# Kernel optimization log

Hardware: AMD Instinct MI355X
Metric: run time of the kernel (lower is better)

Reference implementation:

```python
import jax, jax.numpy as jnp
import numpy as np

B, S, D = 4, 2048, 1024
H, HD = 16, 64
MLP = 4 * D
EPS = 1e-6


def _rms_norm(x, scale):
    var = jnp.mean(jnp.square(x), axis=-1, keepdims=True)
    return x * jax.lax.rsqrt(var + EPS) * scale


def setup_inputs() -> dict:
    key = jax.random.key(0)
    ks = jax.random.split(key, 8)
    sd = D ** -0.5
    return {
        "x": jax.random.normal(ks[0], (B, S, D), jnp.float32),
        "pre_norm_scale": jnp.ones((D,), jnp.float32),
        "w_mlp_in": jax.random.normal(ks[1], (D, MLP), jnp.float32) * sd,   # MLPBlockInput, no bias
        "wq": jax.random.normal(ks[2], (D, H, HD), jnp.float32) * sd,
        "wk": jax.random.normal(ks[3], (D, H, HD), jnp.float32) * sd,
        "wv": jax.random.normal(ks[4], (D, H, HD), jnp.float32) * sd,
        "w_mlp_out": jax.random.normal(ks[5], (MLP, D), jnp.float32) * (MLP ** -0.5),
        "b_mlp_out": jnp.zeros((D,), jnp.float32),
        "w_attn_out": jax.random.normal(ks[6], (H, HD, D), jnp.float32) * sd,  # DenseGeneral axis=(-2,-1)
        "b_attn_out": jnp.zeros((D,), jnp.float32),
    }


def reference(x, pre_norm_scale, w_mlp_in, wq, wk, wv, w_mlp_out, b_mlp_out,
              w_attn_out, b_attn_out):
    residual = x
    xn = _rms_norm(x, pre_norm_scale)                      # pre_norm (TPNorm)

    # QKVMLPDense: fused MLP-input + QKV projections
    h = jax.nn.gelu(jnp.einsum("bsd,df->bsf", xn, w_mlp_in))   # [B,S,MLP]
    q = jnp.einsum("bsd,dhk->bshk", xn, wq)                    # [B,S,H,HD]
    k = jnp.einsum("bsd,dhk->bshk", xn, wk)
    v = jnp.einsum("bsd,dhk->bshk", xn, wv)

    # dot_product_attention (mask=None)
    scores = jnp.einsum("bqhd,bkhd->bhqk", q, k) / jnp.sqrt(jnp.asarray(HD, x.dtype))
    probs = jax.nn.softmax(scores, axis=-1)
    attn_v = jnp.einsum("bhqk,bkhd->bqhd", probs, v)           # [B,S,H,HD]

    # AttnMLPOut: mlp_out + attn_out
    mlp_out = jnp.einsum("bsf,fd->bsd", h, w_mlp_out) + b_mlp_out
    attn_out = jnp.einsum("bqhk,hkd->bqd", attn_v, w_attn_out) + b_attn_out
    block_out = mlp_out + attn_out                              # dropout is identity (train=False)
    return residual + block_out
```

## Files before the change

### kernel.cpp

```cpp
#include <hip/hip_runtime.h>
#include <cstdint>
#include <cstddef>

typedef float floatx4 __attribute__((ext_vector_type(4)));
typedef short bf16x8 __attribute__((ext_vector_type(8)));

#define MFMA(a, b, c) __builtin_amdgcn_mfma_f32_16x16x32_bf16((a), (b), (c), 0, 0, 0)

__device__ __forceinline__ unsigned short f2bf(float f) {
  union { float f; unsigned int u; } v; v.f = f;
  unsigned int u = v.u;
  unsigned int r = (u + 0x7FFFu + ((u >> 16) & 1u)) >> 16;
  return (unsigned short)r;
}

__device__ __forceinline__ void gload_lds16(const unsigned short* g, unsigned short* s) {
  __builtin_amdgcn_global_load_lds(
      (const __attribute__((address_space(1))) unsigned int*)g,
      (__attribute__((address_space(3))) unsigned int*)s, 16, 0, 0);
}

__device__ __forceinline__ float gelu_f(float v) {
  float z = 0.7978845608028654f * (v + 0.044715f * v * v * v);
  float e = __expf(2.0f * z);
  float th = 1.0f - 2.0f / (e + 1.0f);
  return 0.5f * v * (1.0f + th);
}

__global__ __launch_bounds__(256) void prep_all(
    const float* __restrict__ w_mlp_in, const float* __restrict__ wq,
    const float* __restrict__ wk, const float* __restrict__ wv,
    const float* __restrict__ w_mlp_out, const float* __restrict__ w_attn_out,
    const float* __restrict__ x, const float* __restrict__ pns,
    unsigned short* __restrict__ wcatT, unsigned short* __restrict__ wcat2T,
    unsigned short* __restrict__ xn) {
  __shared__ float tile[32][33];
  __shared__ float ws4[4];
  int id = blockIdx.x;
  if (id >= 12288) {
    int row = id - 12288;
    const float4 v = ((const float4*)(x + (size_t)row * 1024))[threadIdx.x];
    float ss = v.x * v.x + v.y * v.y + v.z * v.z + v.w * v.w;
#pragma unroll
    for (int off = 1; off < 64; off <<= 1) ss += __shfl_xor(ss, off, 64);
    if ((threadIdx.x & 63) == 0) ws4[threadIdx.x >> 6] = ss;
    __syncthreads();
    float tot = ws4[0] + ws4[1] + ws4[2] + ws4[3];
    float rs = rsqrtf(tot * (1.0f / 1024.0f) + 1e-6f);
    const float4 sc = ((const float4*)pns)[threadIdx.x];
    uint2 o;
    o.x = (unsigned)f2bf(v.x * rs * sc.x) | ((unsigned)f2bf(v.y * rs * sc.y) << 16);
    o.y = (unsigned)f2bf(v.z * rs * sc.z) | ((unsigned)f2bf(v.w * rs * sc.w) << 16);
    ((uint2*)(xn + (size_t)row * 1024))[threadIdx.x] = o;
    return;
  }
  const float* src; unsigned short* dst; int C, ldd, bx, by, q;
  if (id < 4096)       { src = w_mlp_in;   dst = wcatT;                        C = 4096; ldd = 1024; q = id;         bx = q & 127; by = q >> 7; }
  else if (id < 5120)  { src = wq;         dst = wcatT + (size_t)4096 * 1024;  C = 1024; ldd = 1024; q = id - 4096;  bx = q & 31;  by = q >> 5; }
  else if (id < 6144)  { src = wk;         dst = wcatT + (size_t)5120 * 1024;  C = 1024; ldd = 1024; q = id - 5120;  bx = q & 31;  by = q >> 5; }
  else if (id < 7168)  { src = wv;         dst = wcatT + (size_t)6144 * 1024;  C = 1024; ldd = 1024; q = id - 6144;  bx = q & 31;  by = q >> 5; }
  else if (id < 11264) { src = w_mlp_out;  dst = wcat2T;                       C = 1024; ldd = 5120; q = id - 7168;  bx = q & 31;  by = q >> 5; }
  else                 { src = w_attn_out; dst = wcat2T + 4096;                C = 1024; ldd = 5120; q = id - 11264; bx = q & 31;  by = q >> 5; }
  int tx = threadIdx.x & 31, ty = threadIdx.x >> 5;
#pragma unroll
  for (int i = 0; i < 4; i++) {
    int r = ty + i * 8;
    tile[r][tx] = src[(size_t)(by * 32 + r) * C + bx * 32 + tx];
  }
  __syncthreads();
#pragma unroll
  for (int i = 0; i < 4; i++) {
    int r = ty + i * 8;
    dst[(size_t)(bx * 32 + r) * ldd + by * 32 + tx] = f2bf(tile[tx][r]);
  }
}

template <int MODE>
__device__ __forceinline__ void gemm_core(
    int xcd, int j,
    const unsigned short* __restrict__ A, const unsigned short* __restrict__ BT,
    int K, void* __restrict__ outp,
    const float* __restrict__ bias1, const float* __restrict__ bias2,
    const float* __restrict__ resid,
    int msplit, int tm, int tn,
    unsigned short* __restrict__ q_out, unsigned short* __restrict__ k_out,
    unsigned short* __restrict__ v_out,
    unsigned short* As, unsigned short* Bs) {
  int mh = xcd % msplit, nq = xcd / msplit;
  int by = mh * tm + j / tn;
  int bx = nq * tn + j % tn;
  int m0 = by * 128, n0 = bx * 128;

  int t = threadIdx.x, lane = t & 63, wave = t >> 6;
  int l15 = lane & 15, quad = lane >> 4;
  int wm = (wave & 1) * 64, wn = (wave >> 1) * 64;

  floatx4 acc[4][4] = {};

  int lr = lane >> 2;
  int lg = (lane & 3) ^ ((lane >> 3) & 3);
  int ch0 = wave * 2, ch1 = wave * 2 + 1;
  const unsigned short* gA0 = A + (size_t)(m0 + ch0 * 16 + lr) * K + lg * 8;
  const unsigned short* gA1 = A + (size_t)(m0 + ch1 * 16 + lr) * K + lg * 8;
  const unsigned short* gB0 = BT + (size_t)(n0 + ch0 * 16 + lr) * K + lg * 8;
  const unsigned short* gB1 = BT + (size_t)(n0 + ch1 * 16 + lr) * K + lg * 8;
  unsigned short* sA0[2] = {As + ch0 * 512 + lane * 8, As + 4096 + ch0 * 512 + lane * 8};
  unsigned short* sA1[2] = {As + ch1 * 512 + lane * 8, As + 4096 + ch1 * 512 + lane * 8};
  unsigned short* sB0[2] = {Bs + ch0 * 512 + lane * 8, Bs + 4096 + ch0 * 512 + lane * 8};
  unsigned short* sB1[2] = {Bs + ch1 * 512 + lane * 8, Bs + 4096 + ch1 * 512 + lane * 8};

  int fo = (4 * l15 + (quad ^ ((l15 >> 1) & 3))) * 8;
  int ca = (wm >> 4);
  int cb = (wn >> 4);

  for (int kt = 0; kt < K; kt += 64) {
    __syncthreads();
#pragma unroll
    for (int kk = 0; kk < 2; kk++) {
      int kg = kt + kk * 32;
      gload_lds16(gA0 + kg, sA0[kk]);
      gload_lds16(gA1 + kg, sA1[kk]);
      gload_lds16(gB0 + kg, sB0[kk]);
      gload_lds16(gB1 + kg, sB1[kk]);
    }
    __syncthreads();
#pragma unroll
    for (int kk = 0; kk < 2; kk++) {
      bf16x8 a[4], b[4];
#pragma unroll
      for (int im = 0; im < 4; im++)
        a[im] = *(const bf16x8*)&As[kk * 4096 + (ca + im) * 512 + fo];
#pragma unroll
      for (int in_ = 0; in_ < 4; in_++)
        b[in_] = *(const bf16x8*)&Bs[kk * 4096 + (cb + in_) * 512 + fo];
#pragma unroll
      for (int im = 0; im < 4; im++)
#pragma unroll
        for (int in_ = 0; in_ < 4; in_++)
          acc[im][in_] = MFMA(a[im], b[in_], acc[im][in_]);
    }
  }

#pragma unroll
  for (int im = 0; im < 4; im++) {
#pragma unroll
    for (int in_ = 0; in_ < 4; in_++) {
      int row0 = m0 + wm + im * 16 + quad * 4;
      int col = n0 + wn + in_ * 16 + l15;
      if constexpr (MODE == 8) {
#pragma unroll
        for (int r = 0; r < 4; r++) {
          __builtin_nontemporal_store(f2bf(gelu_f(acc[im][in_][r])),
              &((unsigned short*)outp)[(size_t)(row0 + r) * 5120 + col]);
        }
      } else if constexpr (MODE == 9) {
        int seg = n0 >> 10;
        int cs = col - (seg << 10);
        int h = cs >> 6, hd = cs & 63;
        int b_ = row0 >> 11, s0 = row0 & 2047;
        if (seg == 2) {
          unsigned long long o =
              (unsigned long long)((unsigned)f2bf(acc[im][in_][0]) |
                                   ((unsigned)f2bf(acc[im][in_][1]) << 16)) |
              ((unsigned long long)((unsigned)f2bf(acc[im][in_][2]) |
                                    ((unsigned)f2bf(acc[im][in_][3]) << 16)) << 32);
          __builtin_nontemporal_store(o,
              (unsigned long long*)&v_out[(((size_t)(b_ * 16 + h)) * 64 + hd) * 2048 + s0]);
        } else {
          float sc = (seg == 0) ? 0.125f : 1.0f;
          unsigned short* dst = (seg == 0) ? q_out : k_out;
#pragma unroll
          for (int r = 0; r < 4; r++) {
            __builtin_nontemporal_store(f2bf(acc[im][in_][r] * sc),
                &dst[(((size_t)(b_ * 16 + h)) * 2048 + s0 + r) * 64 + hd]);
          }
        }
      } else {
        float bsum = bias1[col] + bias2[col];
#pragma unroll
        for (int r = 0; r < 4; r++) {
          size_t idx = (size_t)(row0 + r) * 1024 + col;
          float res = __builtin_nontemporal_load(&resid[idx]);
          __builtin_nontemporal_store(acc[im][in_][r] + bsum + res, &((float*)outp)[idx]);
        }
      }
    }
  }
}

template <int MODE>
__global__ __launch_bounds__(256, 2) void gemm_bt(
    const unsigned short* __restrict__ A, const unsigned short* __restrict__ BT,
    int K, void* __restrict__ outp,
    const float* __restrict__ bias1, const float* __restrict__ bias2,
    const float* __restrict__ resid,
    int msplit, int tm, int tn,
    unsigned short* __restrict__ q_out, unsigned short* __restrict__ k_out,
    unsigned short* __restrict__ v_out) {
  __shared__ unsigned short As[2 * 128 * 32];
  __shared__ unsigned short Bs[2 * 128 * 32];
  int id = blockIdx.x + gridDim.x * blockIdx.y;
  gemm_core<MODE>(id & 7, id >> 3, A, BT, K, outp, bias1, bias2, resid,
                  msplit, tm, tn, q_out, k_out, v_out, As, Bs);
}

__device__ __forceinline__ void flash_body(
    int xcd, int j,
    const unsigned short* __restrict__ q_buf, const unsigned short* __restrict__ k_buf,
    const unsigned short* __restrict__ v_buf, unsigned short* __restrict__ cat,
    unsigned short* smem) {
  constexpr int S = 2048, HD = 64;
  constexpr int LK = 72, LV = 72, LP = 68;
  unsigned short* Ks = smem;
  unsigned short* Vs = smem + 4608;
  unsigned short* Psb = smem + 9216;

  int bh = xcd * 8 + (j >> 4);
  int qbk = j & 15;

  int t = threadIdx.x, lane = t & 63, wave = t >> 6;
  int l15 = lane & 15, quad = lane >> 4;
  unsigned short* Ps = Psb + wave * (32 * LP);

  const unsigned short* qp = q_buf + (size_t)bh * S * HD;
  const unsigned short* kp = k_buf + (size_t)bh * S * HD;
  const unsigned short* vp = v_buf + (size_t)bh * HD * S;

  int q0 = qbk * 128 + wave * 32;
  bf16x8 aQ[2][2];
#pragma unroll
  for (int qf = 0; qf < 2; qf++) {
    aQ[qf][0] = *(const bf16x8*)&qp[(size_t)(q0 + qf * 16 + l15) * HD + quad * 8];
    aQ[qf][1] = *(const bf16x8*)&qp[(size_t)(q0 + qf * 16 + l15) * HD + 32 + quad * 8];
  }

  floatx4 acc_o[2][4] = {};
  float lrow[2][4] = {};

  int kr = t >> 3, kc = (t & 7) * 8;

  uint4 rK0 = *(const uint4*)&kp[(size_t)kr * HD + kc];
  uint4 rK1 = *(const uint4*)&kp[(size_t)(kr + 32) * HD + kc];
  uint4 rV0 = *(const uint4*)&vp[(size_t)kr * S + kc];
  uint4 rV1 = *(const uint4*)&vp[(size_t)(kr + 32) * S + kc];

  for (int kv = 0; kv < S; kv += 64) {
    __syncthreads();
    *(uint4*)&Ks[kr * LK + kc] = rK0;
    *(uint4*)&Ks[(kr + 32) * LK + kc] = rK1;
    *(uint4*)&Vs[kr * LV + kc] = rV0;
    *(uint4*)&Vs[(kr + 32) * LV + kc] = rV1;
    __syncthreads();
    if (kv + 64 < S) {
      rK0 = *(const uint4*)&kp[(size_t)(kv + 64 + kr) * HD + kc];
      rK1 = *(const uint4*)&kp[(size_t)(kv + 64 + kr + 32) * HD + kc];
      rV0 = *(const uint4*)&vp[(size_t)kr * S + kv + 64 + kc];
      rV1 = *(const uint4*)&vp[(size_t)(kr + 32) * S + kv + 64 + kc];
    }

    floatx4 z[2][4];
#pragma unroll
    for (int cg = 0; cg < 4; cg++) {
      bf16x8 bk0 = *(const bf16x8*)&Ks[(cg * 16 + l15) * LK + quad * 8];
      bf16x8 bk1 = *(const bf16x8*)&Ks[(cg * 16 + l15) * LK + 32 + quad * 8];
#pragma unroll
      for (int qf = 0; qf < 2; qf++) {
        floatx4 acc = {};
        acc = MFMA(aQ[qf][0], bk0, acc);
        acc = MFMA(aQ[qf][1], bk1, acc);
        z[qf][cg] = acc;
      }
    }
#pragma unroll
    for (int qf = 0; qf < 2; qf++)
#pragma unroll
      for (int cg = 0; cg < 4; cg++)
#pragma unroll
        for (int r = 0; r < 4; r++) {
          float e = __expf(z[qf][cg][r]);
          lrow[qf][r] += e;
          Ps[(qf * 16 + quad * 4 + r) * LP + cg * 16 + l15] = f2bf(e);
        }
    asm volatile("s_waitcnt lgkmcnt(0)" ::: "memory");
#pragma unroll
    for (int c = 0; c < 2; c++) {
      bf16x8 aP[2];
#pragma unroll
      for (int qf = 0; qf < 2; qf++) {
        const unsigned short* pp = &Ps[(qf * 16 + l15) * LP + c * 32 + quad * 8];
        ((uint2*)&aP[qf])[0] = *(const uint2*)pp;
        ((uint2*)&aP[qf])[1] = *(const uint2*)(pp + 4);
      }
#pragma unroll
      for (int n = 0; n < 4; n++) {
        bf16x8 bv = *(const bf16x8*)&Vs[(n * 16 + l15) * LV + c * 32 + quad * 8];
        acc_o[0][n] = MFMA(aP[0], bv, acc_o[0][n]);
        acc_o[1][n] = MFMA(aP[1], bv, acc_o[1][n]);
      }
    }
  }

#pragma unroll
  for (int qf = 0; qf < 2; qf++)
#pragma unroll
    for (int r = 0; r < 4; r++) {
      float s = lrow[qf][r];
#pragma unroll
      for (int off = 1; off < 16; off <<= 1) s += __shfl_xor(s, off, 16);
      lrow[qf][r] = s;
    }

  int b_ = bh >> 4, h = bh & 15;
#pragma unroll
  for (int qf = 0; qf < 2; qf++)
#pragma unroll
    for (int r = 0; r < 4; r++) {
      float inv = 1.0f / lrow[qf][r];
      int srow = q0 + qf * 16 + quad * 4 + r;
      size_t base = ((size_t)(b_ * 2048 + srow)) * 5120 + 4096 + h * 64;
#pragma unroll
      for (int n = 0; n < 4; n++)
        cat[base + n * 16 + l15] = f2bf(acc_o[qf][n][r] * inv);
    }
}

__global__ __launch_bounds__(256, 2) void fused_mlp_attn(
    const unsigned short* __restrict__ xn, const unsigned short* __restrict__ wcatT,
    unsigned short* __restrict__ cat,
    const unsigned short* __restrict__ qb, const unsigned short* __restrict__ kb,
    const unsigned short* __restrict__ vb) {
  __shared__ __align__(16) unsigned short smem[17920];
  int phys = blockIdx.x;
  int xcd = phys & 7, r = phys >> 3;
  if (r % 3 == 2) {
    flash_body(xcd, r / 3, qb, kb, vb, cat, smem);
  } else {
    int g = (r / 3) * 2 + (r % 3);
    gemm_core<8>(xcd, g, xn, wcatT, 1024, cat, nullptr, nullptr, nullptr,
                 2, 32, 8, nullptr, nullptr, nullptr, smem, smem + 8192);
  }
}

extern "C" void kernel_launch(void* const* d_in, const int* in_sizes, int n_in,
                              void* d_out, int out_size, void* d_ws, size_t ws_size,
                              hipStream_t stream) {
  (void)in_sizes; (void)n_in; (void)out_size; (void)ws_size;
  const float* x          = (const float*)d_in[0];
  const float* pns        = (const float*)d_in[1];
  const float* w_mlp_in   = (const float*)d_in[2];
  const float* wq         = (const float*)d_in[3];
  const float* wk         = (const float*)d_in[4];
  const float* wv         = (const float*)d_in[5];
  const float* w_mlp_out  = (const float*)d_in[6];
  const float* b_mlp_out  = (const float*)d_in[7];
  const float* w_attn_out = (const float*)d_in[8];
  const float* b_attn_out = (const float*)d_in[9];
  float* out = (float*)d_out;

  char* ws = (char*)d_ws;
  size_t off = 0;
  auto alloc = [&](size_t bytes) {
    void* p = ws + off;
    off += (bytes + 255) & ~(size_t)255;
    return p;
  };
  const size_t M = 8192;
  unsigned short* xn     = (unsigned short*)alloc(M * 1024 * 2);
  unsigned short* wcatT  = (unsigned short*)alloc((size_t)7168 * 1024 * 2);
  unsigned short* wcat2T = (unsigned short*)alloc((size_t)1024 * 5120 * 2);
  unsigned short* cat    = (unsigned short*)alloc(M * 5120 * 2);
  unsigned short* qb     = (unsigned short*)alloc(M * 1024 * 2);
  unsigned short* kb     = (unsigned short*)alloc(M * 1024 * 2);
  unsigned short* vb     = (unsigned short*)alloc(M * 1024 * 2);

  prep_all<<<dim3(20480), 256, 0, stream>>>(
      w_mlp_in, wq, wk, wv, w_mlp_out, w_attn_out, x, pns, wcatT, wcat2T, xn);

  gemm_bt<9><<<dim3(1536), 256, 0, stream>>>(
      xn, wcatT + (size_t)4096 * 1024, 1024, nullptr, nullptr, nullptr, nullptr,
      2, 32, 6, qb, kb, vb);

  fused_mlp_attn<<<dim3(3072), 256, 0, stream>>>(xn, wcatT, cat, qb, kb, vb);

  gemm_bt<7><<<dim3(8, 64), 256, 0, stream>>>(
      cat, wcat2T, 5120, out, b_mlp_out, b_attn_out, x, 2, 32, 2, nullptr, nullptr, nullptr);
}
```

Measured before the change: 538.6 us.

## Overlap flash attention with MLP-out GEMM and split output GEMM by K

Merges the MLP-in and QKV projections into a single GEMM launch. The fused kernel now runs flash attention alongside the MLP-out GEMM over the first 4096 K columns, writing bias plus residual into the output. A final GEMM then adds the attention-out contribution over the remaining 1024 K columns by read-modify-write of the output. The aim is to hide the attention phase behind the larger MLP GEMM, at the cost of an extra fp32 output read and write pass.

```diff
diff --git a/kernel.cpp b/kernel.cpp
--- a/kernel.cpp
+++ b/kernel.cpp
@@ -79,7 +79,7 @@
 __device__ __forceinline__ void gemm_core(
     int xcd, int j,
     const unsigned short* __restrict__ A, const unsigned short* __restrict__ BT,
-    int K, void* __restrict__ outp,
+    int K, int lda, void* __restrict__ outp,
     const float* __restrict__ bias1, const float* __restrict__ bias2,
     const float* __restrict__ resid,
     int msplit, int tm, int tn,
@@ -100,10 +100,10 @@
   int lr = lane >> 2;
   int lg = (lane & 3) ^ ((lane >> 3) & 3);
   int ch0 = wave * 2, ch1 = wave * 2 + 1;
-  const unsigned short* gA0 = A + (size_t)(m0 + ch0 * 16 + lr) * K + lg * 8;
-  const unsigned short* gA1 = A + (size_t)(m0 + ch1 * 16 + lr) * K + lg * 8;
-  const unsigned short* gB0 = BT + (size_t)(n0 + ch0 * 16 + lr) * K + lg * 8;
-  const unsigned short* gB1 = BT + (size_t)(n0 + ch1 * 16 + lr) * K + lg * 8;
+  const unsigned short* gA0 = A + (size_t)(m0 + ch0 * 16 + lr) * lda + lg * 8;
+  const unsigned short* gA1 = A + (size_t)(m0 + ch1 * 16 + lr) * lda + lg * 8;
+  const unsigned short* gB0 = BT + (size_t)(n0 + ch0 * 16 + lr) * lda + lg * 8;
+  const unsigned short* gB1 = BT + (size_t)(n0 + ch1 * 16 + lr) * lda + lg * 8;
   unsigned short* sA0[2] = {As + ch0 * 512 + lane * 8, As + 4096 + ch0 * 512 + lane * 8};
   unsigned short* sA1[2] = {As + ch1 * 512 + lane * 8, As + 4096 + ch1 * 512 + lane * 8};
   unsigned short* sB0[2] = {Bs + ch0 * 512 + lane * 8, Bs + 4096 + ch0 * 512 + lane * 8};
@@ -147,35 +147,37 @@
     for (int in_ = 0; in_ < 4; in_++) {
       int row0 = m0 + wm + im * 16 + quad * 4;
       int col = n0 + wn + in_ * 16 + l15;
-      if constexpr (MODE == 8) {
-#pragma unroll
-        for (int r = 0; r < 4; r++) {
-          __builtin_nontemporal_store(f2bf(gelu_f(acc[im][in_][r])),
-              &((unsigned short*)outp)[(size_t)(row0 + r) * 5120 + col]);
-        }
-      } else if constexpr (MODE == 9) {
-        int seg = n0 >> 10;
-        int cs = col - (seg << 10);
-        int h = cs >> 6, hd = cs & 63;
-        int b_ = row0 >> 11, s0 = row0 & 2047;
-        if (seg == 2) {
-          unsigned long long o =
-              (unsigned long long)((unsigned)f2bf(acc[im][in_][0]) |
-                                   ((unsigned)f2bf(acc[im][in_][1]) << 16)) |
-              ((unsigned long long)((unsigned)f2bf(acc[im][in_][2]) |
-                                    ((unsigned)f2bf(acc[im][in_][3]) << 16)) << 32);
-          __builtin_nontemporal_store(o,
-              (unsigned long long*)&v_out[(((size_t)(b_ * 16 + h)) * 64 + hd) * 2048 + s0]);
+      if constexpr (MODE == 6) {
+        if (n0 < 4096) {
+#pragma unroll
+          for (int r = 0; r < 4; r++) {
+            __builtin_nontemporal_store(f2bf(gelu_f(acc[im][in_][r])),
+                &((unsigned short*)outp)[(size_t)(row0 + r) * 5120 + col]);
+          }
         } else {
-          float sc = (seg == 0) ? 0.125f : 1.0f;
-          unsigned short* dst = (seg == 0) ? q_out : k_out;
-#pragma unroll
-          for (int r = 0; r < 4; r++) {
-            __builtin_nontemporal_store(f2bf(acc[im][in_][r] * sc),
-                &dst[(((size_t)(b_ * 16 + h)) * 2048 + s0 + r) * 64 + hd]);
+          int seg = (n0 - 4096) >> 10;
+          int cs = col - 4096 - (seg << 10);
+          int h = cs >> 6, hd = cs & 63;
+          int b_ = row0 >> 11, s0 = row0 & 2047;
+          if (seg == 2) {
+            unsigned long long o =
+                (unsigned long long)((unsigned)f2bf(acc[im][in_][0]) |
+                                     ((unsigned)f2bf(acc[im][in_][1]) << 16)) |
+                ((unsigned long long)((unsigned)f2bf(acc[im][in_][2]) |
+                                      ((unsigned)f2bf(acc[im][in_][3]) << 16)) << 32);
+            __builtin_nontemporal_store(o,
+                (unsigned long long*)&v_out[(((size_t)(b_ * 16 + h)) * 64 + hd) * 2048 + s0]);
+          } else {
+            float sc = (seg == 0) ? 0.125f : 1.0f;
+            unsigned short* dst = (seg == 0) ? q_out : k_out;
+#pragma unroll
+            for (int r = 0; r < 4; r++) {
+              __builtin_nontemporal_store(f2bf(acc[im][in_][r] * sc),
+                  &dst[(((size_t)(b_ * 16 + h)) * 2048 + s0 + r) * 64 + hd]);
+            }
           }
         }
-      } else {
+      } else if constexpr (MODE == 10) {
         float bsum = bias1[col] + bias2[col];
 #pragma unroll
         for (int r = 0; r < 4; r++) {
@@ -183,6 +185,13 @@
           float res = __builtin_nontemporal_load(&resid[idx]);
           __builtin_nontemporal_store(acc[im][in_][r] + bsum + res, &((float*)outp)[idx]);
         }
+      } else {
+#pragma unroll
+        for (int r = 0; r < 4; r++) {
+          size_t idx = (size_t)(row0 + r) * 1024 + col;
+          float prev = __builtin_nontemporal_load(&((const float*)outp)[idx]);
+          __builtin_nontemporal_store(prev + acc[im][in_][r], &((float*)outp)[idx]);
+        }
       }
     }
   }
@@ -191,7 +200,7 @@
 template <int MODE>
 __global__ __launch_bounds__(256, 2) void gemm_bt(
     const unsigned short* __restrict__ A, const unsigned short* __restrict__ BT,
-    int K, void* __restrict__ outp,
+    int K, int lda, void* __restrict__ outp,
     const float* __restrict__ bias1, const float* __restrict__ bias2,
     const float* __restrict__ resid,
     int msplit, int tm, int tn,
@@ -200,7 +209,7 @@
   __shared__ unsigned short As[2 * 128 * 32];
   __shared__ unsigned short Bs[2 * 128 * 32];
   int id = blockIdx.x + gridDim.x * blockIdx.y;
-  gemm_core<MODE>(id & 7, id >> 3, A, BT, K, outp, bias1, bias2, resid,
+  gemm_core<MODE>(id & 7, id >> 3, A, BT, K, lda, outp, bias1, bias2, resid,
                   msplit, tm, tn, q_out, k_out, v_out, As, Bs);
 }
 
@@ -324,20 +333,22 @@
     }
 }
 
-__global__ __launch_bounds__(256, 2) void fused_mlp_attn(
-    const unsigned short* __restrict__ xn, const unsigned short* __restrict__ wcatT,
-    unsigned short* __restrict__ cat,
+__global__ __launch_bounds__(256, 2) void fused_attn_mlp(
     const unsigned short* __restrict__ qb, const unsigned short* __restrict__ kb,
-    const unsigned short* __restrict__ vb) {
+    const unsigned short* __restrict__ vb, unsigned short* __restrict__ cat,
+    const unsigned short* __restrict__ wcat2T, float* __restrict__ out,
+    const float* __restrict__ bias1, const float* __restrict__ bias2,
+    const float* __restrict__ resid) {
   __shared__ __align__(16) unsigned short smem[17920];
   int phys = blockIdx.x;
   int xcd = phys & 7, r = phys >> 3;
-  if (r % 3 == 2) {
-    flash_body(xcd, r / 3, qb, kb, vb, cat, smem);
+  if (r % 3 == 0) {
+    gemm_core<10>(xcd, r / 3, cat, wcat2T, 4096, 5120, out,
+                  bias1, bias2, resid, 2, 32, 2,
+                  nullptr, nullptr, nullptr, smem, smem + 8192);
   } else {
-    int g = (r / 3) * 2 + (r % 3);
-    gemm_core<8>(xcd, g, xn, wcatT, 1024, cat, nullptr, nullptr, nullptr,
-                 2, 32, 8, nullptr, nullptr, nullptr, smem, smem + 8192);
+    int j = (r / 3) * 2 + (r % 3 - 1);
+    flash_body(xcd, j, qb, kb, vb, cat, smem);
   }
 }
 
@@ -376,12 +387,13 @@
   prep_all<<<dim3(20480), 256, 0, stream>>>(
       w_mlp_in, wq, wk, wv, w_mlp_out, w_attn_out, x, pns, wcatT, wcat2T, xn);
 
-  gemm_bt<9><<<dim3(1536), 256, 0, stream>>>(
-      xn, wcatT + (size_t)4096 * 1024, 1024, nullptr, nullptr, nullptr, nullptr,
-      2, 32, 6, qb, kb, vb);
-
-  fused_mlp_attn<<<dim3(3072), 256, 0, stream>>>(xn, wcatT, cat, qb, kb, vb);
-
-  gemm_bt<7><<<dim3(8, 64), 256, 0, stream>>>(
-      cat, wcat2T, 5120, out, b_mlp_out, b_attn_out, x, 2, 32, 2, nullptr, nullptr, nullptr);
-}
+  gemm_bt<6><<<dim3(56, 64), 256, 0, stream>>>(
+      xn, wcatT, 1024, 1024, cat, nullptr, nullptr, nullptr, 2, 32, 14, qb, kb, vb);
+
+  fused_attn_mlp<<<dim3(1536), 256, 0, stream>>>(
+      qb, kb, vb, cat, wcat2T, out, b_mlp_out, b_attn_out, x);
+
+  gemm_bt<11><<<dim3(512), 256, 0, stream>>>(
+      cat + 4096, wcat2T + 4096, 1024, 5120, out, nullptr, nullptr, nullptr,
+      2, 32, 2, nullptr, nullptr, nullptr);
+}
```

Measured after the change: 527.9 us. 2.0% less time.
